# Optimization experiments

Measured on AMD Instinct MI355X. Metric: run time of the kernel, lower is better.

## Reference

```python
import jax, jax.numpy as jnp
import numpy as np

EPS = 1e-7      # GENConv message epsilon
BN_EPS = 1e-5   # torch BatchNorm1d eps


def _genconv(x, src, dst, n, w1, b1, gamma, beta, w2, b2):
    # GENConv(aggr='softmax_sg', t=1.0): msg = relu(x_j)+eps, per-feature
    # scatter-softmax weights (stop-grad), weighted sum, residual, MLP
    # [Linear -> BatchNorm(train stats) -> ReLU -> Linear].
    msg = jnp.maximum(x[src], 0.0) + EPS                         # [E, d]
    m = jax.ops.segment_max(msg, dst, num_segments=n)            # [N, d]
    e = jnp.exp(msg - m[dst])
    s = jax.ops.segment_sum(e, dst, num_segments=n)
    alpha = jax.lax.stop_gradient(e / (s[dst] + 1e-16))          # softmax_sg
    agg = jax.ops.segment_sum(msg * alpha, dst, num_segments=n)  # [N, d]
    h = agg + x
    h = h @ w1 + b1
    mu = jnp.mean(h, axis=0)
    var = jnp.var(h, axis=0)
    h = (h - mu) * jax.lax.rsqrt(var + BN_EPS) * gamma + beta
    h = jnp.maximum(h, 0.0)
    return h @ w2 + b2


def _forward(x, edge_index, batch, target,
             g1_w1, g1_b1, g1_g, g1_be, g1_w2, g1_b2,
             g2_w1, g2_b1, g2_g, g2_be, g2_w2, g2_b2,
             g3_w1, g3_b1, g3_g, g3_be, g3_w2, g3_b2,
             fg1_w, fg1_b, fg2_w, fg2_b, fg3_w, fg3_b,
             emb, cw, cb, fxt_w, fxt_b,
             f1_w, f1_b, f2_w, f2_b, o_w, o_b):
    n = x.shape[0]
    nb = target.shape[0]
    src, dst = edge_index[0], edge_index[1]
    h = jnp.maximum(_genconv(x, src, dst, n, g1_w1, g1_b1, g1_g, g1_be, g1_w2, g1_b2), 0.0)
    h = jnp.maximum(_genconv(h, src, dst, n, g2_w1, g2_b1, g2_g, g2_be, g2_w2, g2_b2), 0.0)
    h = jnp.maximum(_genconv(h, src, dst, n, g3_w1, g3_b1, g3_g, g3_be, g3_w2, g3_b2), 0.0)
    # global mean pool over graphs
    sums = jax.ops.segment_sum(h, batch, num_segments=nb)
    cnt = jax.ops.segment_sum(jnp.ones((n, 1), h.dtype), batch, num_segments=nb)
    xg = sums / jnp.maximum(cnt, 1.0)
    xg = jnp.maximum(xg @ fg1_w + fg1_b, 0.0)
    xg = jnp.maximum(xg @ fg2_w + fg2_b, 0.0)
    xg = jnp.maximum(xg @ fg3_w + fg3_b, 0.0)
    # protein branch: embed [B,1000,128], Conv1d(1000->32,k=8) over embed axis
    ext = emb[target]                                            # [B, 1000, 128]
    conv = jax.lax.conv_general_dilated(
        ext, cw, (1,), 'VALID',
        dimension_numbers=('NCW', 'OIW', 'NCW')) + cb[None, :, None]  # [B, 32, 121]
    xt = conv.reshape(nb, 32 * 121) @ fxt_w + fxt_b
    xc = jnp.concatenate([xg, xt], axis=1)                       # [B, 256]
    xc = jnp.maximum(xc @ f1_w + f1_b, 0.0)
    xc = jnp.maximum(xc @ f2_w + f2_b, 0.0)
    return xc @ o_w + o_b


def _lin(k, i, o):
    kw, kb = jax.random.split(k)
    s = 1.0 / np.sqrt(i)
    return (jax.random.uniform(kw, (i, o), jnp.float32, -s, s),
            jax.random.uniform(kb, (o,), jnp.float32, -s, s))


def setup_inputs():
    key = jax.random.key(0)
    ks = jax.random.split(key, 32)
    N, E, B, D = 30000, 150000, 256, 78
    d = {}
    d['x'] = jax.random.normal(ks[0], (N, D), jnp.float32)
    d['edge_index'] = jax.random.randint(ks[1], (2, E), 0, N)
    d['batch'] = jnp.sort(jax.random.randint(ks[2], (N,), 0, B))
    d['target'] = jax.random.randint(ks[3], (B, 1000), 0, 26)
    dims = [(78, 156, 78), (78, 156, 312), (312, 624, 624)]
    for li, (i, hdim, o) in enumerate(dims, start=1):
        w1, b1 = _lin(ks[4 + 2 * li], i, hdim)
        w2, b2 = _lin(ks[5 + 2 * li], hdim, o)
        d['g%d_w1' % li], d['g%d_b1' % li] = w1, b1
        d['g%d_g' % li] = jnp.ones((hdim,), jnp.float32)
        d['g%d_be' % li] = jnp.zeros((hdim,), jnp.float32)
        d['g%d_w2' % li], d['g%d_b2' % li] = w2, b2
    d['fg1_w'], d['fg1_b'] = _lin(ks[14], 624, 512)
    d['fg2_w'], d['fg2_b'] = _lin(ks[15], 512, 1024)
    d['fg3_w'], d['fg3_b'] = _lin(ks[16], 1024, 128)
    d['emb'] = jax.random.normal(ks[17], (26, 128), jnp.float32)
    s = 1.0 / np.sqrt(1000 * 8)
    d['cw'] = jax.random.uniform(ks[18], (32, 1000, 8), jnp.float32, -s, s)
    d['cb'] = jax.random.uniform(ks[19], (32,), jnp.float32, -s, s)
    d['fxt_w'], d['fxt_b'] = _lin(ks[20], 32 * 121, 128)
    d['f1_w'], d['f1_b'] = _lin(ks[21], 256, 1024)
    d['f2_w'], d['f2_b'] = _lin(ks[22], 1024, 512)
    d['o_w'], d['o_b'] = _lin(ks[23], 512, 1)
    return d


def reference(x, edge_index, batch, target,
              g1_w1, g1_b1, g1_g, g1_be, g1_w2, g1_b2,
              g2_w1, g2_b1, g2_g, g2_be, g2_w2, g2_b2,
              g3_w1, g3_b1, g3_g, g3_be, g3_w2, g3_b2,
              fg1_w, fg1_b, fg2_w, fg2_b, fg3_w, fg3_b,
              emb, cw, cb, fxt_w, fxt_b,
              f1_w, f1_b, f2_w, f2_b, o_w, o_b):
    return _forward(x, edge_index, batch, target,
                    g1_w1, g1_b1, g1_g, g1_be, g1_w2, g1_b2,
                    g2_w1, g2_b1, g2_g, g2_be, g2_w2, g2_b2,
                    g3_w1, g3_b1, g3_g, g3_be, g3_w2, g3_b2,
                    fg1_w, fg1_b, fg2_w, fg2_b, fg3_w, fg3_b,
                    emb, cw, cb, fxt_w, fxt_b,
                    f1_w, f1_b, f2_w, f2_b, o_w, o_b)
```

## Files before the change

### kernel.cpp

```cpp
#include <hip/hip_runtime.h>
#include <hip/hip_bf16.h>

typedef unsigned short u16;
typedef __attribute__((ext_vector_type(8))) short bh8;
typedef __attribute__((ext_vector_type(4))) float f32x4;

static __device__ __forceinline__ float b2fu(u16 u) {
    union { float f; unsigned int i; } x;
    x.i = ((unsigned int)u) << 16;
    return x.f;
}
static __device__ __forceinline__ u16 f2bu(float f) {
    __hip_bfloat16 h = __float2bfloat16(f);
    union { __hip_bfloat16 h; u16 u; } x;
    x.h = h;
    return x.u;
}
static __device__ __forceinline__ void load2(const float* p, float& v0, float& v1) {
    float2 v = *reinterpret_cast<const float2*>(p);
    v0 = v.x; v1 = v.y;
}
static __device__ __forceinline__ void load2(const u16* p, float& v0, float& v1) {
    unsigned int u = *reinterpret_cast<const unsigned int*>(p);
    v0 = b2fu((u16)(u & 0xffff)); v1 = b2fu((u16)(u >> 16));
}


__global__ __launch_bounds__(256) void const_out_kernel(float* __restrict__ out, float v, int n) {
    int i = blockIdx.x * 256 + threadIdx.x;
    if (i < n) out[i] = v;
}


__global__ __launch_bounds__(256) void hist_kernel(const int* __restrict__ dst,
                                                   int* __restrict__ hist, int E) {
    int e = blockIdx.x * 256 + threadIdx.x;
    if (e < E) atomicAdd(&hist[dst[e]], 1);
}

__global__ __launch_bounds__(256) void scan_kernel(const int* __restrict__ hist,
                                                   int* __restrict__ rowptr,
                                                   int* __restrict__ fill, int N) {
    __shared__ int csum[256];
    __shared__ int coff[257];
    int t = threadIdx.x;
    int chunk = (N + 255) / 256;
    int lo = min(t * chunk, N), hi = min(lo + chunk, N);
    int s = 0;
    for (int i = lo; i < hi; i++) s += hist[i];
    csum[t] = s;
    __syncthreads();
    if (t == 0) {
        int acc = 0;
        for (int i = 0; i < 256; i++) { coff[i] = acc; acc += csum[i]; }
        rowptr[N] = acc;
    }
    __syncthreads();
    int run = coff[t];
    for (int i = lo; i < hi; i++) {
        rowptr[i] = run;
        fill[i] = run;
        run += hist[i];
    }
}

__global__ __launch_bounds__(256) void scan_tiles(const int* __restrict__ hist, int N,
                                                  int* __restrict__ rowptr,
                                                  int* __restrict__ tsum) {
    int tid = threadIdx.x;
    int i = blockIdx.x * 256 + tid;
    int v = (i < N) ? hist[i] : 0;
    __shared__ int s[256];
    s[tid] = v;
    __syncthreads();
    for (int off = 1; off < 256; off <<= 1) {
        int t = (tid >= off) ? s[tid - off] : 0;
        __syncthreads();
        s[tid] += t;
        __syncthreads();
    }
    if (i < N) rowptr[i] = s[tid] - v;
    if (tid == 255) tsum[blockIdx.x] = s[255];
}

__global__ __launch_bounds__(256) void scan_tsum(const int* __restrict__ tsum, int ntiles,
                                                 int* __restrict__ toff,
                                                 int* __restrict__ totalp) {
    int tid = threadIdx.x;
    int v = (tid < ntiles) ? tsum[tid] : 0;
    __shared__ int s[256];
    s[tid] = v;
    __syncthreads();
    for (int off = 1; off < 256; off <<= 1) {
        int t = (tid >= off) ? s[tid - off] : 0;
        __syncthreads();
        s[tid] += t;
        __syncthreads();
    }
    if (tid < ntiles) toff[tid] = s[tid] - v;
    if (tid == 255) *totalp = s[255];
}

__global__ __launch_bounds__(256) void scan_apply(int* __restrict__ rowptr,
                                                  const int* __restrict__ toff, int N,
                                                  int* __restrict__ fill) {
    int i = blockIdx.x * 256 + threadIdx.x;
    if (i < N) {
        int r = rowptr[i] + toff[blockIdx.x];
        rowptr[i] = r;
        fill[i] = r;
    }
}

__global__ __launch_bounds__(256) void scatter_kernel(const int* __restrict__ src,
                                                      const int* __restrict__ dst,
                                                      int* __restrict__ fill,
                                                      int* __restrict__ srcs, int E) {
    int e = blockIdx.x * 256 + threadIdx.x;
    if (e < E) {
        int p = atomicAdd(&fill[dst[e]], 1);
        srcs[p] = src[e];
    }
}


template <typename T>
__global__ __launch_bounds__(256) void agg_kernel(const T* __restrict__ x,
                                                  const int* __restrict__ rowptr,
                                                  const int* __restrict__ srcs,
                                                  u16* __restrict__ out, int d, int Kp, int N) {
    int n = blockIdx.y * 4 + (threadIdx.x >> 6);
    int f = (blockIdx.x * 64 + (threadIdx.x & 63)) * 2;
    if (n >= N || f >= Kp) return;
    size_t o = (size_t)n * Kp + f;
    if (f >= d) {
        *reinterpret_cast<unsigned int*>(out + o) = 0;
        return;
    }
    int e0 = rowptr[n], e1 = rowptr[n + 1];
    float s0 = 0.f, t0 = 0.f, s1 = 0.f, t1 = 0.f;
    for (int e = e0; e < e1; e++) {
        int sr = srcs[e];
        float v0, v1;
        load2(x + (size_t)sr * d + f, v0, v1);
        float m0 = fmaxf(v0, 0.f) + 1e-7f;
        float w0 = __expf(m0);
        s0 += w0; t0 += m0 * w0;
        float m1 = fmaxf(v1, 0.f) + 1e-7f;
        float w1 = __expf(m1);
        s1 += w1; t1 += m1 * w1;
    }
    float x0, x1;
    load2(x + (size_t)n * d + f, x0, x1);
    float a0 = t0 / (s0 + 1e-16f) + x0;
    float a1 = t1 / (s1 + 1e-16f) + x1;
    unsigned int pk = (unsigned int)f2bu(a0) | ((unsigned int)f2bu(a1) << 16);
    *reinterpret_cast<unsigned int*>(out + o) = pk;
}


__global__ __launch_bounds__(256) void wt_cvt(const float* __restrict__ W, int K, int N,
                                              u16* __restrict__ WT, int Kp, int Np) {
    int n = blockIdx.y * 4 + (threadIdx.x >> 6);
    int k = blockIdx.x * 64 + (threadIdx.x & 63);
    if (n >= Np || k >= Kp) return;
    float v = (n < N && k < K) ? W[(size_t)k * N + n] : 0.f;
    WT[(size_t)n * Kp + k] = f2bu(v);
}


__global__ __launch_bounds__(256) void cvt_bn(const u16* __restrict__ H,
                                              const float* __restrict__ scale,
                                              const float* __restrict__ shift,
                                              u16* __restrict__ out, int dh, int Kp, int M) {
    int m = blockIdx.y * 4 + (threadIdx.x >> 6);
    int f = blockIdx.x * 64 + (threadIdx.x & 63);
    if (m >= M || f >= Kp) return;
    size_t o = (size_t)m * Kp + f;
    if (f >= dh) { out[o] = 0; return; }
    float v = fmaxf(fmaf(b2fu(H[(size_t)m * dh + f]), scale[f], shift[f]), 0.f);
    out[o] = f2bu(v);
}


template <bool RELU, typename CT>
__global__ __launch_bounds__(256) void gemm_mfma(const u16* __restrict__ A,
                                                 const u16* __restrict__ BT,
                                                 const float* __restrict__ bias,
                                                 CT* __restrict__ C, int ldc, int M, int Ncols,
                                                 int Kp, int nbx, int nby, int spx) {
    int xcd = blockIdx.x & 7;
    int j = blockIdx.x >> 3;
    int bx = j % nbx;
    int by = xcd * spx + j / nbx;
    if (by >= nby) return;
    __shared__ u16 As[2][128 * 40];
    __shared__ u16 Bs[2][128 * 40];
    const int tid = threadIdx.x;
    const int lane = tid & 63;
    const int w = tid >> 6;
    const int bm = by * 128;
    const int bn = bx * 128;
    f32x4 acc[4][4] = {};
    const int srow = tid >> 1;
    const int spart = tid & 1;
    const u16* Ag = A + (size_t)(bm + srow) * Kp + spart * 16;
    const u16* Bg = BT + (size_t)(bn + srow) * Kp + spart * 16;
    const int swoff = srow * 40 + spart * 16;
    const int fm = (w >> 1) * 64 + (lane & 15);
    const int fn = (w & 1) * 64 + (lane & 15);
    const int fk = (lane >> 4) * 8;

    uint4 a0 = *reinterpret_cast<const uint4*>(Ag);
    uint4 a1 = *reinterpret_cast<const uint4*>(Ag + 8);
    uint4 b0 = *reinterpret_cast<const uint4*>(Bg);
    uint4 b1 = *reinterpret_cast<const uint4*>(Bg + 8);
    *reinterpret_cast<uint4*>(&As[0][swoff]) = a0;
    *reinterpret_cast<uint4*>(&As[0][swoff + 8]) = a1;
    *reinterpret_cast<uint4*>(&Bs[0][swoff]) = b0;
    *reinterpret_cast<uint4*>(&Bs[0][swoff + 8]) = b1;

    const int nk = Kp >> 5;
    for (int k = 0; k < nk; k++) {
        const int cur = k & 1;
        const int nxt = cur ^ 1;
        if (k + 1 < nk) {
            int off = (k + 1) << 5;
            a0 = *reinterpret_cast<const uint4*>(Ag + off);
            a1 = *reinterpret_cast<const uint4*>(Ag + off + 8);
            b0 = *reinterpret_cast<const uint4*>(Bg + off);
            b1 = *reinterpret_cast<const uint4*>(Bg + off + 8);
        }
        __syncthreads();
        bh8 af[4], bf[4];
#pragma unroll
        for (int mt = 0; mt < 4; mt++)
            af[mt] = *reinterpret_cast<const bh8*>(&As[cur][(fm + mt * 16) * 40 + fk]);
#pragma unroll
        for (int nt = 0; nt < 4; nt++)
            bf[nt] = *reinterpret_cast<const bh8*>(&Bs[cur][(fn + nt * 16) * 40 + fk]);
#pragma unroll
        for (int mt = 0; mt < 4; mt++)
#pragma unroll
            for (int nt = 0; nt < 4; nt++)
                acc[mt][nt] = __builtin_amdgcn_mfma_f32_16x16x32_bf16(af[mt], bf[nt],
                                                                      acc[mt][nt], 0, 0, 0);
        if (k + 1 < nk) {
            *reinterpret_cast<uint4*>(&As[nxt][swoff]) = a0;
            *reinterpret_cast<uint4*>(&As[nxt][swoff + 8]) = a1;
            *reinterpret_cast<uint4*>(&Bs[nxt][swoff]) = b0;
            *reinterpret_cast<uint4*>(&Bs[nxt][swoff + 8]) = b1;
        }
    }
    const int rq = (lane >> 4) * 4;
    const int cl = lane & 15;
#pragma unroll
    for (int mt = 0; mt < 4; mt++) {
#pragma unroll
        for (int nt = 0; nt < 4; nt++) {
            int n = bn + (w & 1) * 64 + nt * 16 + cl;
            if (n >= Ncols) continue;
            float bv = bias[n];
#pragma unroll
            for (int r = 0; r < 4; r++) {
                int m = bm + (w >> 1) * 64 + mt * 16 + rq + r;
                if (m >= M) continue;
                float v = acc[mt][nt][r] + bv;
                if (RELU) v = fmaxf(v, 0.f);
                if (sizeof(CT) == 2)
                    C[(size_t)m * ldc + n] = (CT)f2bu(v);
                else
                    C[(size_t)m * ldc + n] = (CT)v;
            }
        }
    }
}


__global__ __launch_bounds__(256) void bn_stats(const u16* __restrict__ H, int N, int dh,
                                                float* __restrict__ sum,
                                                float* __restrict__ sumsq) {
    int col = blockIdx.x * 64 + (threadIdx.x & 63);
    int rl = threadIdx.x >> 6;
    int rowsPerBlock = (N + gridDim.y - 1) / gridDim.y;
    int r0 = blockIdx.y * rowsPerBlock;
    int r1 = min(r0 + rowsPerBlock, N);
    float s0 = 0.f, s1 = 0.f;
    if (col < dh) {
        for (int r = r0 + rl; r < r1; r += 4) {
            float v = b2fu(H[(size_t)r * dh + col]);
            s0 += v;
            s1 += v * v;
        }
    }
    __shared__ float ls0[4][64];
    __shared__ float ls1[4][64];
    ls0[rl][threadIdx.x & 63] = s0;
    ls1[rl][threadIdx.x & 63] = s1;
    __syncthreads();
    if (rl == 0 && col < dh) {
        int c = threadIdx.x & 63;
        atomicAdd(&sum[col], ls0[0][c] + ls0[1][c] + ls0[2][c] + ls0[3][c]);
        atomicAdd(&sumsq[col], ls1[0][c] + ls1[1][c] + ls1[2][c] + ls1[3][c]);
    }
}

__global__ __launch_bounds__(256) void bn_final(const float* __restrict__ sum,
                                                const float* __restrict__ sumsq,
                                                const float* __restrict__ gamma,
                                                const float* __restrict__ beta,
                                                float* __restrict__ scale,
                                                float* __restrict__ shift, int dh, float invN) {
    int i = blockIdx.x * 256 + threadIdx.x;
    if (i < dh) {
        float mu = sum[i] * invN;
        float var = sumsq[i] * invN - mu * mu;
        float sc = gamma[i] / sqrtf(var + 1e-5f);
        scale[i] = sc;
        shift[i] = beta[i] - mu * sc;
    }
}


__global__ __launch_bounds__(256) void pool_seg(const u16* __restrict__ h,
                                                const int* __restrict__ goff,
                                                float* __restrict__ gsum, int d) {
    int g = blockIdx.y;
    int c = threadIdx.x & 63;
    int f = blockIdx.x * 64 + c;
    int wv = threadIdx.x >> 6;
    int r0 = goff[g], r1 = goff[g + 1];
    float s = 0.f;
    if (f < d)
        for (int r = r0 + wv; r < r1; r += 4) s += b2fu(h[(size_t)r * d + f]);
    __shared__ float ls[4][64];
    ls[wv][c] = s;
    __syncthreads();
    if (wv == 0 && f < d) {
        float tot = ls[0][c] + ls[1][c] + ls[2][c] + ls[3][c];
        gsum[(size_t)g * d + f] = tot / fmaxf((float)(r1 - r0), 1.f);
    }
}


__global__ __launch_bounds__(256) void gemm_sk(const float* __restrict__ A, int lda,
                                               const float* __restrict__ B, int ldb,
                                               float* __restrict__ C, int ldc, int M, int K,
                                               int Nn, int KC) {
    __shared__ float As[16][17];
    __shared__ float Bs[16][68];
    const int tid = threadIdx.x;
    const int bn = blockIdx.x * 64;
    const int bm = blockIdx.y * 16;
    const int k0 = blockIdx.z * KC;
    const int kend = min(K, k0 + KC);
    const int tx = tid & 63;
    const int ty = tid >> 6;
    float acc[4] = {};
    const int am = bm + (tid >> 4);
    const int ak = tid & 15;
    for (int kk0 = k0; kk0 < kend; kk0 += 16) {
        {
            int k = kk0 + ak;
            As[ak][tid >> 4] = (am < M && k < kend) ? A[(size_t)am * lda + k] : 0.f;
        }
#pragma unroll
        for (int i = 0; i < 4; i++) {
            int k = kk0 + ty + 4 * i;
            Bs[ty + 4 * i][tx] = (k < kend && bn + tx < Nn) ? B[(size_t)k * ldb + bn + tx] : 0.f;
        }
        __syncthreads();
#pragma unroll
        for (int kk = 0; kk < 16; kk++) {
            float b = Bs[kk][tx];
#pragma unroll
            for (int i = 0; i < 4; i++) acc[i] = fmaf(As[kk][ty + 4 * i], b, acc[i]);
        }
        __syncthreads();
    }
    if (bn + tx < Nn) {
#pragma unroll
        for (int i = 0; i < 4; i++) {
            int m = bm + ty + 4 * i;
            if (m < M) atomicAdd(&C[(size_t)m * ldc + bn + tx], acc[i]);
        }
    }
}

__global__ __launch_bounds__(256) void bias_act(float* __restrict__ C, int ldc,
                                                const float* __restrict__ bias, int M, int Nn,
                                                int relu) {
    int idx = blockIdx.x * 256 + threadIdx.x;
    if (idx >= M * Nn) return;
    int m = idx / Nn, n = idx - m * Nn;
    float v = C[(size_t)m * ldc + n] + bias[n];
    C[(size_t)m * ldc + n] = relu ? fmaxf(v, 0.f) : v;
}

static void launch_gemm_small(const float* A, int lda, const float* B, int ldb,
                              const float* bias, float* C, int ldc, int M, int K, int Nn,
                              bool relu, hipStream_t stream) {
    int gx = (Nn + 63) / 64, gy = (M + 15) / 16;
    int tiles = gx * gy;
    int ksplit = 512 / tiles;
    if (ksplit < 1) ksplit = 1;
    int maxsplit = (K + 63) / 64;
    if (ksplit > maxsplit) ksplit = maxsplit;
    int KC = (((K + ksplit - 1) / ksplit) + 15) & ~15;
    ksplit = (K + KC - 1) / KC;
    gemm_sk<<<dim3(gx, gy, ksplit), 256, 0, stream>>>(A, lda, B, ldb, C, ldc, M, K, Nn, KC);
    bias_act<<<(M * Nn + 255) / 256, 256, 0, stream>>>(C, ldc, bias, M, Nn, relu ? 1 : 0);
}


__global__ __launch_bounds__(256) void hone_kernel(const int* __restrict__ target,
                                                   u16* __restrict__ H, int total) {
    int i = blockIdx.x * 256 + threadIdx.x;
    if (i >= total) return;
    int b = i / 1000, pos = i - b * 1000;
    int t = target[i];
    H[((size_t)b * 26 + t) * 1024 + pos] = 0x3F80;
}

__global__ __launch_bounds__(256) void cwt_cvt(const float* __restrict__ cw,
                                               u16* __restrict__ BT) {
    int n = blockIdx.y;
    int kk = blockIdx.x * 256 + threadIdx.x;
    int o = n >> 3, k = n & 7;
    float v = (kk < 1000) ? cw[(size_t)o * 8000 + (size_t)kk * 8 + k] : 0.f;
    BT[(size_t)n * 1024 + kk] = f2bu(v);
}

__global__ __launch_bounds__(256) void prot_conv_kernel(const float* __restrict__ S,
                                                        const float* __restrict__ emb,
                                                        const float* __restrict__ cb,
                                                        float* __restrict__ out) {
    int b = blockIdx.x;
    int tid = threadIdx.x;
    __shared__ float Sl[6656];
    __shared__ float el[26 * 128];
    for (int i = tid; i < 6656; i += 256) Sl[i] = S[(size_t)b * 6656 + i];
    for (int i = tid; i < 26 * 128; i += 256) el[i] = emb[i];
    __syncthreads();
    for (int j = tid; j < 3872; j += 256) {
        int o = j / 121;
        int w = j - o * 121;
        float acc = cb[o];
        for (int t = 0; t < 26; t++) {
#pragma unroll
            for (int k = 0; k < 8; k++)
                acc = fmaf(Sl[t * 256 + o * 8 + k], el[t * 128 + w + k], acc);
        }
        out[(size_t)b * 3872 + j] = acc;
    }
}


__global__ __launch_bounds__(256) void out_kernel(const float* __restrict__ A,
                                                  const float* __restrict__ w,
                                                  const float* __restrict__ bias,
                                                  float* __restrict__ out, int M, int K) {
    int wave = threadIdx.x >> 6;
    int lane = threadIdx.x & 63;
    int r = blockIdx.x * 4 + wave;
    if (r >= M) return;
    float acc = 0.f;
    for (int k = lane; k < K; k += 64) acc += A[(size_t)r * K + k] * w[k];
    for (int off = 32; off > 0; off >>= 1) acc += __shfl_down(acc, off, 64);
    if (lane == 0) out[r] = acc + bias[0];
}


static inline int KP(int k) { return (k + 31) & ~31; }
static inline int NP(int n) { return (n + 127) & ~127; }

extern "C" void kernel_launch(void* const* d_in, const int* in_sizes, int n_in, void* d_out,
                              int out_size, void* d_ws, size_t ws_size, hipStream_t stream) {
    static const int exp_sizes[39] = {
        2340000, 300000, 30000, 256000,
        12168, 156, 156, 156, 12168, 78,
        12168, 156, 156, 156, 48672, 312,
        194688, 624, 624, 624, 389376, 624,
        319488, 512, 524288, 1024, 131072, 128,
        3328, 256000, 32, 495616, 128,
        262144, 1024, 524288, 512, 512, 1};
    int bad = (n_in != 39) ? 100 : -1;
    if (bad < 0)
        for (int i = 0; i < 39; i++)
            if (in_sizes[i] != exp_sizes[i]) { bad = i; break; }
    if (bad >= 0) {
        const_out_kernel<<<1, 256, 0, stream>>>((float*)d_out, 2048.f + 8.f * bad, out_size);
        return;
    }

    const int N = 30000, E = 150000, B = 256;
    const int Mp = 30080;
    const int nby = 235, spx = 30;
    const int ntiles = (N + 255) / 256;
    const float* x_in = (const float*)d_in[0];
    const int* ei = (const int*)d_in[1];
    const int* src = ei;
    const int* dst = ei + E;
    const int* batch = (const int*)d_in[2];
    const int* target = (const int*)d_in[3];

    char* p = (char*)d_ws;
    auto carve = [&](size_t bytes) {
        char* r = p;
        p += (bytes + 15) & ~(size_t)15;
        return r;
    };
    int* hist = (int*)carve((size_t)(N + B) * 4);
    int* ghist = hist + N;
    int* rowptr = (int*)carve((size_t)(N + 1) * 4);
    int* fill = (int*)carve((size_t)N * 4);
    int* srcs = (int*)carve((size_t)E * 4);
    int* goff = (int*)carve((size_t)(B + 1) * 4);
    int* gfill = (int*)carve((size_t)B * 4);
    int* tsum = (int*)carve(256 * 4);
    int* toff = (int*)carve(256 * 4);
    float* sum_ = (float*)carve(2 * 624 * 4);
    float* sumsq_ = sum_ + 624;
    float* scale_ = (float*)carve(624 * 4);
    float* shift_ = (float*)carve(624 * 4);
    float* zero256 = (float*)carve(256 * 4);
    float* gsum = (float*)carve((size_t)B * 624 * 4);
    float* fc1 = (float*)carve((size_t)B * 512 * 4);
    float* fc2 = (float*)carve((size_t)B * 1024 * 4);
    float* xc = (float*)carve((size_t)B * 256 * 4);
    float* fcc1 = (float*)carve((size_t)B * 1024 * 4);
    float* fcc2 = (float*)carve((size_t)B * 512 * 4);
    float* Sbuf = (float*)carve((size_t)B * 6656 * 4);
    float* convb = (float*)carve((size_t)B * 3872 * 4);
    u16* Hbuf = (u16*)carve((size_t)B * 26 * 1024 * 2);
    u16* cwT = (u16*)carve((size_t)256 * 1024 * 2);
    u16* Abf = (u16*)carve((size_t)Mp * 640 * 2);
    u16* hmidb = (u16*)carve((size_t)N * 624 * 2);
    u16* Lout = (u16*)carve((size_t)N * 624 * 2);
    struct Layer { int di, dh, dn, w1, b1, g, be, w2, b2; };
    const Layer L[3] = {
        {78, 156, 78, 4, 5, 6, 7, 8, 9},
        {78, 156, 312, 10, 11, 12, 13, 14, 15},
        {312, 624, 624, 16, 17, 18, 19, 20, 21},
    };
    u16* WT1[3];
    u16* WT2[3];
    for (int li = 0; li < 3; li++) {
        WT1[li] = (u16*)carve((size_t)NP(L[li].dh) * KP(L[li].di) * 2);
        WT2[li] = (u16*)carve((size_t)NP(L[li].dn) * KP(L[li].dh) * 2);
    }
    size_t need = (size_t)(p - (char*)d_ws);
    if (ws_size < need) {
        const_out_kernel<<<1, 256, 0, stream>>>((float*)d_out,
                                                1024.f + (float)(ws_size >> 20), out_size);
        return;
    }

    hipMemsetAsync(hist, 0, (size_t)(N + B) * 4, stream);
    hipMemsetAsync(zero256, 0, 256 * 4, stream);
    hist_kernel<<<(E + 255) / 256, 256, 0, stream>>>(dst, hist, E);
    hist_kernel<<<(N + 255) / 256, 256, 0, stream>>>(batch, ghist, N);
    scan_tiles<<<ntiles, 256, 0, stream>>>(hist, N, rowptr, tsum);
    scan_tsum<<<1, 256, 0, stream>>>(tsum, ntiles, toff, rowptr + N);
    scan_apply<<<ntiles, 256, 0, stream>>>(rowptr, toff, N, fill);
    scan_kernel<<<1, 256, 0, stream>>>(ghist, goff, gfill, B);
    scatter_kernel<<<(E + 255) / 256, 256, 0, stream>>>(src, dst, fill, srcs, E);

    for (int li = 0; li < 3; li++) {
        int Kp1 = KP(L[li].di), Np1 = NP(L[li].dh);
        int Kp2 = KP(L[li].dh), Np2 = NP(L[li].dn);
        wt_cvt<<<dim3((Kp1 + 63) / 64, Np1 / 4), 256, 0, stream>>>(
            (const float*)d_in[L[li].w1], L[li].di, L[li].dh, WT1[li], Kp1, Np1);
        wt_cvt<<<dim3((Kp2 + 63) / 64, Np2 / 4), 256, 0, stream>>>(
            (const float*)d_in[L[li].w2], L[li].dh, L[li].dn, WT2[li], Kp2, Np2);
    }

    for (int li = 0; li < 3; li++) {
        const int di = L[li].di, dh = L[li].dh, dn = L[li].dn;
        const int Kp1 = KP(di), Kp2 = KP(dh);
        if (li == 0)
            agg_kernel<float><<<dim3((Kp1 / 2 + 63) / 64, (N + 3) / 4), 256, 0, stream>>>(
                x_in, rowptr, srcs, Abf, di, Kp1, N);
        else
            agg_kernel<u16><<<dim3((Kp1 / 2 + 63) / 64, (N + 3) / 4), 256, 0, stream>>>(
                Lout, rowptr, srcs, Abf, di, Kp1, N);
        {
            int nbx = NP(dh) / 128;
            gemm_mfma<false, u16><<<dim3(8 * spx * nbx), 256, 0, stream>>>(
                Abf, WT1[li], (const float*)d_in[L[li].b1], hmidb, dh, N, dh, Kp1, nbx, nby,
                spx);
        }
        hipMemsetAsync(sum_, 0, 2 * 624 * 4, stream);
        bn_stats<<<dim3((dh + 63) / 64, 60), 256, 0, stream>>>(hmidb, N, dh, sum_, sumsq_);
        bn_final<<<(dh + 255) / 256, 256, 0, stream>>>(sum_, sumsq_, (const float*)d_in[L[li].g],
                                                       (const float*)d_in[L[li].be], scale_,
                                                       shift_, dh, 1.0f / N);
        cvt_bn<<<dim3((Kp2 + 63) / 64, (N + 3) / 4), 256, 0, stream>>>(hmidb, scale_, shift_,
                                                                       Abf, dh, Kp2, N);
        {
            int nbx = NP(dn) / 128;
            gemm_mfma<true, u16><<<dim3(8 * spx * nbx), 256, 0, stream>>>(
                Abf, WT2[li], (const float*)d_in[L[li].b2], Lout, dn, N, dn, Kp2, nbx, nby,
                spx);
        }
    }

    pool_seg<<<dim3(10, B), 256, 0, stream>>>(Lout, goff, gsum, 624);

    hipMemsetAsync(fc1, 0, (size_t)B * 3328 * 4, stream);

    launch_gemm_small(gsum, 624, (const float*)d_in[22], 512, (const float*)d_in[23], fc1, 512,
                      B, 624, 512, true, stream);
    launch_gemm_small(fc1, 512, (const float*)d_in[24], 1024, (const float*)d_in[25], fc2, 1024,
                      B, 512, 1024, true, stream);
    launch_gemm_small(fc2, 1024, (const float*)d_in[26], 128, (const float*)d_in[27], xc, 256,
                      B, 1024, 128, true, stream);

    hipMemsetAsync(Hbuf, 0, (size_t)B * 26 * 1024 * 2, stream);
    hone_kernel<<<(B * 1000 + 255) / 256, 256, 0, stream>>>(target, Hbuf, B * 1000);
    cwt_cvt<<<dim3(4, 256), 256, 0, stream>>>((const float*)d_in[29], cwT);
    {
        int nbxS = 2, nbyS = 52, spxS = 7;
        gemm_mfma<false, float><<<dim3(8 * spxS * nbxS), 256, 0, stream>>>(
            Hbuf, cwT, zero256, Sbuf, 256, 6656, 256, 1024, nbxS, nbyS, spxS);
    }
    prot_conv_kernel<<<B, 256, 0, stream>>>(Sbuf, (const float*)d_in[28],
                                            (const float*)d_in[30], convb);
    launch_gemm_small(convb, 3872, (const float*)d_in[31], 128, (const float*)d_in[32],
                      xc + 128, 256, B, 3872, 128, false, stream);

    launch_gemm_small(xc, 256, (const float*)d_in[33], 1024, (const float*)d_in[34], fcc1, 1024,
                      B, 256, 1024, true, stream);
    launch_gemm_small(fcc1, 1024, (const float*)d_in[35], 512, (const float*)d_in[36], fcc2, 512,
                      B, 1024, 512, true, stream);
    out_kernel<<<(B + 3) / 4, 256, 0, stream>>>(fcc2, (const float*)d_in[37],
                                                (const float*)d_in[38], (float*)d_out, B, 512);
}
```

Before: 923.4 us.

## Use direct global-to-LDS loads with triple buffering in bf16 MFMA GEMM

Replaces the register-staged double-buffered tile loads in the MFMA GEMM with `global_load_lds` direct-to-LDS copies and a three-stage ring buffer, tracked by explicit vmcnt waits and raw barriers. The LDS row padding is dropped in favour of an XOR swizzle on the k-chunk index so fragment reads avoid bank conflicts. The intent is to cut VGPR pressure and the LDS store instructions, and to keep two tiles of loads in flight while MFMAs run. The hand-written waitcnt counts and barrier placement are fragile: if they do not match the number of outstanding loads, the kernel reads stale data.

```diff
diff --git a/kernel.cpp b/kernel.cpp
--- a/kernel.cpp
+++ b/kernel.cpp
@@ -23,6 +23,12 @@
 static __device__ __forceinline__ void load2(const u16* p, float& v0, float& v1) {
     unsigned int u = *reinterpret_cast<const unsigned int*>(p);
     v0 = b2fu((u16)(u & 0xffff)); v1 = b2fu((u16)(u >> 16));
+}
+
+static __device__ __forceinline__ void gload16(const u16* g, u16* l) {
+    __builtin_amdgcn_global_load_lds(
+        (const __attribute__((address_space(1))) unsigned int*)(const void*)g,
+        (__attribute__((address_space(3))) unsigned int*)(void*)l, 16, 0, 0);
 }
 
 
@@ -194,63 +200,70 @@
     int bx = j % nbx;
     int by = xcd * spx + j / nbx;
     if (by >= nby) return;
-    __shared__ u16 As[2][128 * 40];
-    __shared__ u16 Bs[2][128 * 40];
+    __shared__ u16 As[3][128 * 32];
+    __shared__ u16 Bs[3][128 * 32];
     const int tid = threadIdx.x;
     const int lane = tid & 63;
     const int w = tid >> 6;
     const int bm = by * 128;
     const int bn = bx * 128;
     f32x4 acc[4][4] = {};
-    const int srow = tid >> 1;
-    const int spart = tid & 1;
-    const u16* Ag = A + (size_t)(bm + srow) * Kp + spart * 16;
-    const u16* Bg = BT + (size_t)(bn + srow) * Kp + spart * 16;
-    const int swoff = srow * 40 + spart * 16;
+
+    const int r0 = w * 16 + (lane >> 2);
+    const int r1 = r0 + 64;
+    const int sw = ((lane & 3) ^ ((r0 >> 1) & 3)) << 3;
+    const u16* Ag0 = A + (size_t)(bm + r0) * Kp + sw;
+    const u16* Ag1 = A + (size_t)(bm + r1) * Kp + sw;
+    const u16* Bg0 = BT + (size_t)(bn + r0) * Kp + sw;
+    const u16* Bg1 = BT + (size_t)(bn + r1) * Kp + sw;
+    const int wb = w << 9;
+
+    auto stage = [&](int b, int koff) {
+        gload16(Ag0 + koff, &As[b][wb]);
+        gload16(Ag1 + koff, &As[b][2048 + wb]);
+        gload16(Bg0 + koff, &Bs[b][wb]);
+        gload16(Bg1 + koff, &Bs[b][2048 + wb]);
+    };
+
     const int fm = (w >> 1) * 64 + (lane & 15);
     const int fn = (w & 1) * 64 + (lane & 15);
-    const int fk = (lane >> 4) * 8;
-
-    uint4 a0 = *reinterpret_cast<const uint4*>(Ag);
-    uint4 a1 = *reinterpret_cast<const uint4*>(Ag + 8);
-    uint4 b0 = *reinterpret_cast<const uint4*>(Bg);
-    uint4 b1 = *reinterpret_cast<const uint4*>(Bg + 8);
-    *reinterpret_cast<uint4*>(&As[0][swoff]) = a0;
-    *reinterpret_cast<uint4*>(&As[0][swoff + 8]) = a1;
-    *reinterpret_cast<uint4*>(&Bs[0][swoff]) = b0;
-    *reinterpret_cast<uint4*>(&Bs[0][swoff + 8]) = b1;
+    const int g = lane >> 4;
+    const int ka = (g ^ ((fm >> 1) & 3)) << 3;
+    const int kb = (g ^ ((fn >> 1) & 3)) << 3;
 
     const int nk = Kp >> 5;
+    stage(0, 0);
+    if (nk > 1) stage(1, 32);
+    int cur = 0, stg = 2;
     for (int k = 0; k < nk; k++) {
-        const int cur = k & 1;
-        const int nxt = cur ^ 1;
-        if (k + 1 < nk) {
-            int off = (k + 1) << 5;
-            a0 = *reinterpret_cast<const uint4*>(Ag + off);
-            a1 = *reinterpret_cast<const uint4*>(Ag + off + 8);
-            b0 = *reinterpret_cast<const uint4*>(Bg + off);
-            b1 = *reinterpret_cast<const uint4*>(Bg + off + 8);
-        }
-        __syncthreads();
+        if (k + 2 < nk) stage(stg, (k + 2) << 5);
+        if (k + 2 < nk)
+            asm volatile("s_waitcnt vmcnt(8)" ::: "memory");
+        else if (k + 1 < nk)
+            asm volatile("s_waitcnt vmcnt(4)" ::: "memory");
+        else
+            asm volatile("s_waitcnt vmcnt(0)" ::: "memory");
+        __builtin_amdgcn_sched_barrier(0);
+        __builtin_amdgcn_s_barrier();
+        __builtin_amdgcn_sched_barrier(0);
         bh8 af[4], bf[4];
 #pragma unroll
         for (int mt = 0; mt < 4; mt++)
-            af[mt] = *reinterpret_cast<const bh8*>(&As[cur][(fm + mt * 16) * 40 + fk]);
+            af[mt] = *reinterpret_cast<const bh8*>(&As[cur][(fm + mt * 16) * 32 + ka]);
 #pragma unroll
         for (int nt = 0; nt < 4; nt++)
-            bf[nt] = *reinterpret_cast<const bh8*>(&Bs[cur][(fn + nt * 16) * 40 + fk]);
+            bf[nt] = *reinterpret_cast<const bh8*>(&Bs[cur][(fn + nt * 16) * 32 + kb]);
+        asm volatile("s_waitcnt lgkmcnt(0)" ::: "memory");
+        __builtin_amdgcn_sched_barrier(0);
+        __builtin_amdgcn_s_barrier();
 #pragma unroll
         for (int mt = 0; mt < 4; mt++)
 #pragma unroll
             for (int nt = 0; nt < 4; nt++)
                 acc[mt][nt] = __builtin_amdgcn_mfma_f32_16x16x32_bf16(af[mt], bf[nt],
                                                                       acc[mt][nt], 0, 0, 0);
-        if (k + 1 < nk) {
-            *reinterpret_cast<uint4*>(&As[nxt][swoff]) = a0;
-            *reinterpret_cast<uint4*>(&As[nxt][swoff + 8]) = a1;
-            *reinterpret_cast<uint4*>(&Bs[nxt][swoff]) = b0;
-            *reinterpret_cast<uint4*>(&Bs[nxt][swoff + 8]) = b1;
-        }
+        cur = (cur == 2) ? 0 : cur + 1;
+        stg = (stg == 2) ? 0 : stg + 1;
     }
     const int rq = (lane >> 4) * 4;
     const int cl = lane & 15;
```

Result: slower. 950.9 us (+3.0%).
